# Optimization experiments

Hardware: AMD Instinct MI355X
Metric: run time of the kernel (lower is better)

Reference implementation:

```python
import jax, jax.numpy as jnp
import numpy as np

N, E, Q = 50000, 800000, 2000000   # nodes, edges, quadruplets
F_IN, H, OUT, G = 128, 128, 1, 64  # in_channels, hidden, out_channels, graphs
NRBF = NCBF = NSBF = 6
L = 3  # num_layers


def _mlp2(h, Wa, ba, Wb, bb):
    # Linear -> ReLU -> Linear
    return jax.nn.relu(h @ Wa + ba) @ Wb + bb


def setup_inputs() -> dict:
    key = jax.random.key(0)
    ks = jax.random.split(key, 24)
    s = 0.05
    inp = {
        "x": jax.random.normal(ks[0], (N, F_IN), jnp.float32),
        "rbf": jax.random.normal(ks[1], (E, NRBF), jnp.float32),
        "cbf": jax.random.normal(ks[2], (Q, NCBF), jnp.float32),
        "sbf": jax.random.normal(ks[3], (Q, NSBF), jnp.float32),
        "edge_index": jax.random.randint(ks[4], (2, E), 0, N),
        "l_idx": jax.random.randint(ks[5], (Q,), 0, N),
        "k_idx": jax.random.randint(ks[6], (Q,), 0, E),
        "batch": jnp.sort(jax.random.randint(ks[7], (N,), 0, G)),
        # per-layer params (all layers share shapes since F_IN == H)
        "W_e1a": s * jax.random.normal(ks[8], (L, F_IN + NRBF + NCBF + NSBF, H)),
        "b_e1a": jnp.zeros((L, H)),
        "W_e1b": s * jax.random.normal(ks[9], (L, H, H)),
        "b_e1b": jnp.zeros((L, H)),
        "W_e2a": s * jax.random.normal(ks[10], (L, 2 * H, H)),
        "b_e2a": jnp.zeros((L, H)),
        "W_e2b": s * jax.random.normal(ks[11], (L, H, H)),
        "b_e2b": jnp.zeros((L, H)),
        "W_na": s * jax.random.normal(ks[12], (L, F_IN + H, H)),
        "b_na": jnp.zeros((L, H)),
        "W_nb": s * jax.random.normal(ks[13], (L, H, H)),
        "b_nb": jnp.zeros((L, H)),
        "W_oa": s * jax.random.normal(ks[14], (H, H)),
        "b_oa": jnp.zeros((H,)),
        "W_ob": s * jax.random.normal(ks[15], (H, OUT)),
        "b_ob": jnp.zeros((OUT,)),
    }
    return inp


def reference(x, rbf, cbf, sbf,
              W_e1a, b_e1a, W_e1b, b_e1b,
              W_e2a, b_e2a, W_e2b, b_e2b,
              W_na, b_na, W_nb, b_nb,
              W_oa, b_oa, W_ob, b_ob,
              edge_index, l_idx, k_idx, batch):
    src, dst = edge_index[0], edge_index[1]  # x_j = x[src], index = dst
    h = x
    for p in range(L):
        # quadruplet message: gather-concat-MLP  [Q, F+18] -> [Q, H]
        m_in = jnp.concatenate([h[l_idx], rbf[k_idx], cbf, sbf], axis=-1)
        em = _mlp2(m_in, W_e1a[p], b_e1a[p], W_e1b[p], b_e1b[p])
        # scatter-add quadruplet messages onto edges by k_idx -> [E, H]
        agg_e = jax.ops.segment_sum(em, k_idx, num_segments=E)
        # second stage: per-edge concat (note: aggregated indexed by dst, as in source)
        fin = jnp.concatenate([h[src], agg_e[dst]], axis=-1)
        msg = _mlp2(fin, W_e2a[p], b_e2a[p], W_e2b[p], b_e2b[p])
        # aggregate edge messages to target nodes -> [N, H]
        aggr = jax.ops.segment_sum(msg, dst, num_segments=N)
        h = _mlp2(jnp.concatenate([h, aggr], axis=-1), W_na[p], b_na[p], W_nb[p], b_nb[p])
    # global mean pool over graphs
    counts = jax.ops.segment_sum(jnp.ones((N, 1), h.dtype), batch, num_segments=G)
    pooled = jax.ops.segment_sum(h, batch, num_segments=G) / jnp.maximum(counts, 1.0)
    pooled = jax.nn.relu(pooled)
    return _mlp2(pooled, W_oa, b_oa, W_ob, b_ob)
```

## Files before the change

kernel.cpp:

```cpp
#include <hip/hip_runtime.h>

constexpr int Nn = 50000;
constexpr int Ee = 800000;
constexpr int Qq = 2000000;
constexpr int Gg = 64;
constexpr int Hh = 128;
constexpr int NB64 = (Nn + 63) / 64;
constexpr int NSCB = (Nn + 1023) / 1024;

typedef short bf16x8 __attribute__((ext_vector_type(8)));
typedef float f32x4  __attribute__((ext_vector_type(4)));

__device__ __forceinline__ unsigned short f2bf(float f) {
    unsigned u = __builtin_bit_cast(unsigned, f);
    u += 0x7FFFu + ((u >> 16) & 1u);
    return (unsigned short)(u >> 16);
}
__device__ __forceinline__ float bf2f(unsigned short s) {
    unsigned u = ((unsigned)s) << 16;
    return __builtin_bit_cast(float, u);
}

__global__ void k_hist(const int* __restrict__ idx, int n, int limit,
                       int* __restrict__ hist) {
    int i = blockIdx.x * blockDim.x + threadIdx.x;
    if (i < n) { int v = idx[i]; if (v < limit) atomicAdd(&hist[v], 1); }
}

__global__ __launch_bounds__(1024) void k_scanA(const int* __restrict__ hist,
                                                int* __restrict__ cursor,
                                                int* __restrict__ bsum) {
    __shared__ int s[1024];
    const int tid = threadIdx.x;
    int i = blockIdx.x * 1024 + tid;
    int v = (i < Nn) ? hist[i] : 0;
    s[tid] = v;
    __syncthreads();
    for (int off = 1; off < 1024; off <<= 1) {
        int t = (tid >= off) ? s[tid - off] : 0;
        __syncthreads();
        s[tid] += t;
        __syncthreads();
    }
    if (i < Nn) cursor[i] = s[tid] - v;
    if (tid == 1023) bsum[blockIdx.x] = s[1023];
}
__global__ void k_scanB(int* __restrict__ bsum) {
    __shared__ int s[64];
    const int tid = threadIdx.x;
    int v = (tid < NSCB) ? bsum[tid] : 0;
    s[tid] = v;
    __syncthreads();
    for (int off = 1; off < 64; off <<= 1) {
        int t = (tid >= off) ? s[tid - off] : 0;
        __syncthreads();
        s[tid] += t;
        __syncthreads();
    }
    if (tid < NSCB) bsum[tid] = s[tid] - v;
}
__global__ __launch_bounds__(1024) void k_scanC(int* __restrict__ cursor,
                                                const int* __restrict__ bsum) {
    int i = blockIdx.x * 1024 + threadIdx.x;
    if (i < Nn) cursor[i] += bsum[blockIdx.x];
}

__global__ void k_scatter_e(const int* __restrict__ dst, const int* __restrict__ src,
                            int* __restrict__ cursor, int* __restrict__ srcs) {
    int i = blockIdx.x * blockDim.x + threadIdx.x;
    if (i < Ee) {
        int v = dst[i];
        int p = atomicAdd(&cursor[v], 1);
        srcs[p] = src[i];
    }
}

__global__ void k_scatter_q(const int* __restrict__ k_idx, const int* __restrict__ l_idx,
                            const float* __restrict__ cbf, const float* __restrict__ sbf,
                            int* __restrict__ cursor,
                            int* __restrict__ lq, unsigned short* __restrict__ qfeat) {
    int i = blockIdx.x * blockDim.x + threadIdx.x;
    if (i >= Qq) return;
    int v = k_idx[i];
    if (v >= Nn) return;
    int p = atomicAdd(&cursor[v], 1);
    lq[p] = l_idx[i];
    unsigned short f[12];
#pragma unroll
    for (int k = 0; k < 6; ++k) f[k] = f2bf(cbf[(size_t)i * 6 + k]);
#pragma unroll
    for (int k = 0; k < 6; ++k) f[6 + k] = f2bf(sbf[(size_t)i * 6 + k]);
    *(uint2*)&qfeat[(size_t)p * 12]     = *(uint2*)&f[0];
    *(uint2*)&qfeat[(size_t)p * 12 + 4] = *(uint2*)&f[4];
    *(uint2*)&qfeat[(size_t)p * 12 + 8] = *(uint2*)&f[8];
}

__global__ void k_wtall(const float* __restrict__ We1a0, const float* __restrict__ We1b0,
                        const float* __restrict__ We2a0, const float* __restrict__ We2b0,
                        const float* __restrict__ Wna0,  const float* __restrict__ Wnb0,
                        unsigned short* __restrict__ wbuf) {
    int idx = blockIdx.x * blockDim.x + threadIdx.x;
    if (idx >= 135168) return;
    const int p = blockIdx.y;
    const float* We1a = We1a0 + (size_t)p * 146 * 128;
    const float* We1b = We1b0 + (size_t)p * 128 * 128;
    const float* We2a = We2a0 + (size_t)p * 256 * 128;
    const float* We2b = We2b0 + (size_t)p * 128 * 128;
    const float* Wna  = Wna0  + (size_t)p * 256 * 128;
    const float* Wnb  = Wnb0  + (size_t)p * 128 * 128;
    unsigned short* base = wbuf + (size_t)p * 135168;
    const float* src; int K, Kp, loc;
    if (idx < 16384)       { src = We1a;             K = 128; Kp = 128; loc = idx; }
    else if (idx < 20480)  { src = We1a + 128 * 128; K = 6;   Kp = 32;  loc = idx - 16384; }
    else if (idx < 36864)  { src = We1b;             K = 128; Kp = 128; loc = idx - 20480; }
    else if (idx < 69632)  { src = We2a;             K = 256; Kp = 256; loc = idx - 36864; }
    else if (idx < 86016)  { src = We2b;             K = 128; Kp = 128; loc = idx - 69632; }
    else if (idx < 118784) { src = Wna;              K = 256; Kp = 256; loc = idx - 86016; }
    else                   { src = Wnb;              K = 128; Kp = 128; loc = idx - 118784; }
    int n = loc / Kp, k = loc - n * Kp;
    base[idx] = (k < K) ? f2bf(src[(size_t)k * 128 + n]) : (unsigned short)0;
}

__global__ void k_h0(const float* __restrict__ x, unsigned short* __restrict__ hb) {
    int idx = blockIdx.x * blockDim.x + threadIdx.x;
    if (idx < Nn * Hh) hb[idx] = f2bf(x[idx]);
}

__device__ __forceinline__ void zacc(f32x4 acc[4][2]) {
#pragma unroll
    for (int rt = 0; rt < 4; ++rt)
#pragma unroll
        for (int ct = 0; ct < 2; ++ct)
            acc[rt][ct] = (f32x4){0.f, 0.f, 0.f, 0.f};
}

template<int KK, int SA, int KP>
__device__ __forceinline__ void gemm64(const unsigned short* A,
                                       const unsigned short* __restrict__ Wt,
                                       int k_off, f32x4 acc[4][2]) {
    const int tid = threadIdx.x;
    const int lane = tid & 63;
    const int nb = (tid >> 6) * 32;
    const int rA = lane & 15;
    const int kg = lane >> 4;
#pragma unroll
    for (int ks = 0; ks < KK / 32; ++ks) {
        const int ka = ks * 32 + kg * 8;
        const int kb = k_off + ka;
        bf16x8 b0 = *(const bf16x8*)&Wt[(size_t)(nb + rA) * KP + kb];
        bf16x8 b1 = *(const bf16x8*)&Wt[(size_t)(nb + 16 + rA) * KP + kb];
#pragma unroll
        for (int rt = 0; rt < 4; ++rt) {
            bf16x8 a = *(const bf16x8*)&A[(rt * 16 + rA) * SA + ka];
            acc[rt][0] = __builtin_amdgcn_mfma_f32_16x16x32_bf16(a, b0, acc[rt][0], 0, 0, 0);
            acc[rt][1] = __builtin_amdgcn_mfma_f32_16x16x32_bf16(a, b1, acc[rt][1], 0, 0, 0);
        }
    }
}

__device__ __forceinline__ void store_acc(const f32x4 acc[4][2], unsigned short* out,
                                          int n0, int nmax) {
    const int tid = threadIdx.x;
    const int lane = tid & 63;
    const int nb = (tid >> 6) * 32;
    const int rA = lane & 15, kg = lane >> 4;
#pragma unroll
    for (int rt = 0; rt < 4; ++rt)
#pragma unroll
        for (int ct = 0; ct < 2; ++ct) {
            int col = nb + ct * 16 + rA;
#pragma unroll
            for (int i = 0; i < 4; ++i) {
                int n = n0 + rt * 16 + kg * 4 + i;
                if (n < nmax) out[(size_t)n * 128 + col] = f2bf(acc[rt][ct][i]);
            }
        }
}

__global__ __launch_bounds__(256) void k_pre(
    const unsigned short* __restrict__ hb, const float* __restrict__ rbf,
    const unsigned short* __restrict__ wb,
    unsigned short* __restrict__ P1, unsigned short* __restrict__ Z1,
    unsigned short* __restrict__ P2)
{
    __shared__ unsigned short L[64 * 136];
    const int m0 = blockIdx.x * 64;
    const int tid = threadIdx.x;
    const unsigned short* Wq1t = wb;
    const unsigned short* Wp2t = wb + 16384;
    const unsigned short* We2at = wb + 36864;
    for (int i = tid; i < 64 * 16; i += 256) {
        int row = i >> 4, ch = i & 15;
        int n = min(m0 + row, Nn - 1);
        *(uint4*)&L[row * 136 + ch * 8] = *(const uint4*)&hb[(size_t)n * 128 + ch * 8];
    }
    __syncthreads();
    f32x4 acc[4][2];
    zacc(acc);
    gemm64<128, 136, 128>(L, Wq1t, 0, acc);
    store_acc(acc, P1, m0, Nn);
    zacc(acc);
    gemm64<128, 136, 256>(L, We2at, 0, acc);
    store_acc(acc, Z1, m0, Nn);
    __syncthreads();
    for (int i = tid; i < 64 * 32; i += 256) {
        int row = i >> 5, c = i & 31;
        int n = min(m0 + row, Nn - 1);
        float v = (c < 6) ? rbf[(size_t)n * 6 + c] : 0.f;
        L[row * 136 + c] = f2bf(v);
    }
    __syncthreads();
    zacc(acc);
    gemm64<32, 136, 32>(L, Wp2t, 0, acc);
    store_acc(acc, P2, m0, Nn);
}

__global__ __launch_bounds__(256) void k_quadagg(
    const unsigned short* __restrict__ P1, const unsigned short* __restrict__ P2,
    const unsigned short* __restrict__ qfeat, const int* __restrict__ lq,
    const int* __restrict__ rowend, const int* __restrict__ rowcnt,
    const float* __restrict__ We1a_raw, const float* __restrict__ b_e1a,
    unsigned short* __restrict__ Rb)
{
    __shared__ float W34[12 * 128];
    __shared__ float bia[128];
    const int tid = threadIdx.x;
    for (int i = tid; i < 12 * 128; i += 256) W34[i] = We1a_raw[134 * 128 + i];
    if (tid < 128) bia[tid] = b_e1a[tid];
    __syncthreads();
    const int nd = tid >> 4;
    const int c0 = (tid & 15) * 8;
    const int n = blockIdx.x * 16 + nd;
    const int end = rowend[n];
    const int beg = end - rowcnt[n];
    float base[8];
    {
        uint4 p2v = *(const uint4*)&P2[(size_t)n * 128 + c0];
        const unsigned short* pp = (const unsigned short*)&p2v;
#pragma unroll
        for (int k = 0; k < 8; ++k) base[k] = bia[c0 + k] + bf2f(pp[k]);
    }
    float acc[8];
#pragma unroll
    for (int k = 0; k < 8; ++k) acc[k] = 0.f;
    for (int e = beg; e < end; ++e) {
        int l = lq[e];
        uint4 a = *(const uint4*)&P1[(size_t)l * 128 + c0];
        uint2 f0 = *(const uint2*)&qfeat[(size_t)e * 12];
        uint2 f1 = *(const uint2*)&qfeat[(size_t)e * 12 + 4];
        uint2 f2 = *(const uint2*)&qfeat[(size_t)e * 12 + 8];
        const unsigned short* q0 = (const unsigned short*)&f0;
        const unsigned short* q1 = (const unsigned short*)&f1;
        const unsigned short* q2 = (const unsigned short*)&f2;
        float qv[12] = {bf2f(q0[0]), bf2f(q0[1]), bf2f(q0[2]), bf2f(q0[3]),
                        bf2f(q1[0]), bf2f(q1[1]), bf2f(q1[2]), bf2f(q1[3]),
                        bf2f(q2[0]), bf2f(q2[1]), bf2f(q2[2]), bf2f(q2[3])};
        const unsigned short* ap = (const unsigned short*)&a;
        float t[8];
#pragma unroll
        for (int k = 0; k < 8; ++k) t[k] = base[k] + bf2f(ap[k]);
#pragma unroll
        for (int kk = 0; kk < 12; ++kk) {
            float q_ = qv[kk];
#pragma unroll
            for (int k = 0; k < 8; ++k)
                t[k] = fmaf(q_, W34[kk * 128 + c0 + k], t[k]);
        }
#pragma unroll
        for (int k = 0; k < 8; ++k) acc[k] += fmaxf(t[k], 0.f);
    }
    unsigned short ov[8];
#pragma unroll
    for (int k = 0; k < 8; ++k) ov[k] = f2bf(acc[k]);
    *(uint4*)&Rb[(size_t)n * 128 + c0] = *(uint4*)ov;
}

__global__ __launch_bounds__(256) void k_edgeagg(
    const unsigned short* __restrict__ Z1, const unsigned short* __restrict__ Z2,
    const int* __restrict__ srcs,
    const int* __restrict__ rowend, const int* __restrict__ rowcnt,
    const float* __restrict__ b_e2a,
    unsigned short* __restrict__ Rb)
{
    const int tid = threadIdx.x;
    const int nd = tid >> 4;
    const int c0 = (tid & 15) * 8;
    const int n = blockIdx.x * 16 + nd;
    const int end = rowend[n];
    const int beg = end - rowcnt[n];
    float z2b[8];
    {
        uint4 zv = *(const uint4*)&Z2[(size_t)n * 128 + c0];
        const unsigned short* zp = (const unsigned short*)&zv;
        float4 b0 = *(const float4*)&b_e2a[c0];
        float4 b1 = *(const float4*)&b_e2a[c0 + 4];
        z2b[0] = b0.x + bf2f(zp[0]); z2b[1] = b0.y + bf2f(zp[1]);
        z2b[2] = b0.z + bf2f(zp[2]); z2b[3] = b0.w + bf2f(zp[3]);
        z2b[4] = b1.x + bf2f(zp[4]); z2b[5] = b1.y + bf2f(zp[5]);
        z2b[6] = b1.z + bf2f(zp[6]); z2b[7] = b1.w + bf2f(zp[7]);
    }
    float acc[8];
#pragma unroll
    for (int k = 0; k < 8; ++k) acc[k] = 0.f;
    int e = beg;
    for (; e + 2 <= end; e += 2) {
        int s0 = srcs[e], s1 = srcs[e + 1];
        uint4 a0 = *(const uint4*)&Z1[(size_t)s0 * 128 + c0];
        uint4 a1 = *(const uint4*)&Z1[(size_t)s1 * 128 + c0];
        const unsigned short* p0 = (const unsigned short*)&a0;
        const unsigned short* p1 = (const unsigned short*)&a1;
#pragma unroll
        for (int k = 0; k < 8; ++k) acc[k] += fmaxf(z2b[k] + bf2f(p0[k]), 0.f);
#pragma unroll
        for (int k = 0; k < 8; ++k) acc[k] += fmaxf(z2b[k] + bf2f(p1[k]), 0.f);
    }
    if (e < end) {
        int s0 = srcs[e];
        uint4 a0 = *(const uint4*)&Z1[(size_t)s0 * 128 + c0];
        const unsigned short* p0 = (const unsigned short*)&a0;
#pragma unroll
        for (int k = 0; k < 8; ++k) acc[k] += fmaxf(z2b[k] + bf2f(p0[k]), 0.f);
    }
    unsigned short ov[8];
#pragma unroll
    for (int k = 0; k < 8; ++k) ov[k] = f2bf(acc[k]);
    *(uint4*)&Rb[(size_t)n * 128 + c0] = *(uint4*)ov;
}

__global__ __launch_bounds__(256) void k_agg2z(
    const unsigned short* __restrict__ Rb, const int* __restrict__ cntq,
    const unsigned short* __restrict__ wb, const float* __restrict__ b_e1b,
    unsigned short* __restrict__ Z2)
{
    __shared__ unsigned short L[64 * 136];
    __shared__ int rc[64];
    const int m0 = blockIdx.x * 64;
    const int tid = threadIdx.x;
    const unsigned short* We1bt = wb + 20480;
    const unsigned short* We2at = wb + 36864;
    if (tid < 64) rc[tid] = (m0 + tid < Nn) ? cntq[m0 + tid] : 0;
    for (int i = tid; i < 64 * 16; i += 256) {
        int row = i >> 4, ch = i & 15;
        int n = min(m0 + row, Nn - 1);
        *(uint4*)&L[row * 136 + ch * 8] = *(const uint4*)&Rb[(size_t)n * 128 + ch * 8];
    }
    __syncthreads();
    f32x4 acc[4][2];
    zacc(acc);
    gemm64<128, 136, 128>(L, We1bt, 0, acc);
    __syncthreads();
    {
        const int lane = tid & 63;
        const int nb = (tid >> 6) * 32;
        const int rA = lane & 15, kg = lane >> 4;
#pragma unroll
        for (int rt = 0; rt < 4; ++rt)
#pragma unroll
            for (int ct = 0; ct < 2; ++ct) {
                int col = nb + ct * 16 + rA;
                float bias = b_e1b[col];
#pragma unroll
                for (int i = 0; i < 4; ++i) {
                    int row = rt * 16 + kg * 4 + i;
                    L[row * 136 + col] = f2bf(acc[rt][ct][i] + (float)rc[row] * bias);
                }
            }
    }
    __syncthreads();
    zacc(acc);
    gemm64<128, 136, 256>(L, We2at, 128, acc);
    store_acc(acc, Z2, m0, Nn);
}

__global__ __launch_bounds__(256) void k_nodeNew(
    const unsigned short* __restrict__ Rb, const int* __restrict__ deg,
    const unsigned short* __restrict__ wb,
    const float* __restrict__ b_e2b, const float* __restrict__ b_na,
    const float* __restrict__ b_nb,
    unsigned short* __restrict__ hb)
{
    __shared__ unsigned short L[64 * 136];
    __shared__ int rc[64];
    const int m0 = blockIdx.x * 64;
    const int tid = threadIdx.x;
    const unsigned short* We2bt = wb + 69632;
    const unsigned short* Wnat  = wb + 86016;
    const unsigned short* Wnbt  = wb + 118784;
    const int lane = tid & 63;
    const int nb = (tid >> 6) * 32;
    const int rA = lane & 15, kg = lane >> 4;
    if (tid < 64) rc[tid] = (m0 + tid < Nn) ? deg[m0 + tid] : 0;
    for (int i = tid; i < 64 * 16; i += 256) {
        int row = i >> 4, ch = i & 15;
        int n = min(m0 + row, Nn - 1);
        *(uint4*)&L[row * 136 + ch * 8] = *(const uint4*)&Rb[(size_t)n * 128 + ch * 8];
    }
    __syncthreads();
    f32x4 acc[4][2];
    zacc(acc);
    gemm64<128, 136, 128>(L, We2bt, 0, acc);
    __syncthreads();
#pragma unroll
    for (int rt = 0; rt < 4; ++rt)
#pragma unroll
        for (int ct = 0; ct < 2; ++ct) {
            int col = nb + ct * 16 + rA;
            float bias = b_e2b[col];
#pragma unroll
            for (int i = 0; i < 4; ++i) {
                int row = rt * 16 + kg * 4 + i;
                L[row * 136 + col] = f2bf(acc[rt][ct][i] + (float)rc[row] * bias);
            }
        }
    __syncthreads();
    f32x4 acc2[4][2];
    zacc(acc2);
    gemm64<128, 136, 256>(L, Wnat, 128, acc2);
    __syncthreads();
    for (int i = tid; i < 64 * 16; i += 256) {
        int row = i >> 4, ch = i & 15;
        int n = min(m0 + row, Nn - 1);
        *(uint4*)&L[row * 136 + ch * 8] = *(const uint4*)&hb[(size_t)n * 128 + ch * 8];
    }
    __syncthreads();
    gemm64<128, 136, 256>(L, Wnat, 0, acc2);
    __syncthreads();
#pragma unroll
    for (int rt = 0; rt < 4; ++rt)
#pragma unroll
        for (int ct = 0; ct < 2; ++ct) {
            int col = nb + ct * 16 + rA;
            float bias = b_na[col];
#pragma unroll
            for (int i = 0; i < 4; ++i) {
                int row = rt * 16 + kg * 4 + i;
                L[row * 136 + col] = f2bf(fmaxf(acc2[rt][ct][i] + bias, 0.f));
            }
        }
    __syncthreads();
    zacc(acc);
    gemm64<128, 136, 128>(L, Wnbt, 0, acc);
#pragma unroll
    for (int rt = 0; rt < 4; ++rt)
#pragma unroll
        for (int ct = 0; ct < 2; ++ct) {
            int col = nb + ct * 16 + rA;
            float bias = b_nb[col];
#pragma unroll
            for (int i = 0; i < 4; ++i) {
                int n = m0 + rt * 16 + kg * 4 + i;
                if (n < Nn)
                    hb[(size_t)n * 128 + col] = f2bf(acc[rt][ct][i] + bias);
            }
        }
}

__global__ __launch_bounds__(256) void k_pool(const unsigned short* __restrict__ hb,
                                              const int* __restrict__ batch,
                                              float* __restrict__ pooled,
                                              float* __restrict__ cntg) {
    __shared__ int bseg[200];
    constexpr int CH = 196;
    const int start = blockIdx.x * CH;
    const int end = min(start + CH, Nn);
    if (start >= end) return;
    const int tid = threadIdx.x;
    for (int i = tid; i < end - start; i += 256) bseg[i] = batch[start + i];
    __syncthreads();
    const int j = tid & 127;
    const int rh = tid >> 7;
    float acc = 0.f, cacc = 0.f;
    int cur = -1;
    for (int n = start + rh; n < end; n += 2) {
        int g = bseg[n - start];
        if (g != cur) {
            if (cur >= 0) {
                atomicAdd(&pooled[cur * Hh + j], acc);
                if (j == 0) atomicAdd(&cntg[cur], cacc);
            }
            cur = g; acc = 0.f; cacc = 0.f;
        }
        acc += bf2f(hb[(size_t)n * Hh + j]);
        cacc += 1.f;
    }
    if (cur >= 0) {
        atomicAdd(&pooled[cur * Hh + j], acc);
        if (j == 0) atomicAdd(&cntg[cur], cacc);
    }
}

__global__ __launch_bounds__(128) void k_final(
    const float* __restrict__ pooled, const float* __restrict__ cntg,
    const float* __restrict__ Woa, const float* __restrict__ boa,
    const float* __restrict__ Wob, const float* __restrict__ bob,
    float* __restrict__ out)
{
    __shared__ float p[128];
    __shared__ float t[128];
    __shared__ float red[128];
    const int g = blockIdx.x;
    const int j = threadIdx.x;
    float c = fmaxf(cntg[g], 1.f);
    p[j] = fmaxf(pooled[g * Hh + j] / c, 0.f);
    __syncthreads();
    float acc = boa[j];
    for (int d = 0; d < Hh; ++d) acc = fmaf(p[d], Woa[d * Hh + j], acc);
    t[j] = fmaxf(acc, 0.f);
    __syncthreads();
    red[j] = t[j] * Wob[j];
    __syncthreads();
    for (int s = 64; s > 0; s >>= 1) {
        if (j < s) red[j] += red[j + s];
        __syncthreads();
    }
    if (j == 0) out[g] = red[0] + bob[0];
}

extern "C" void kernel_launch(void* const* d_in, const int* in_sizes, int n_in,
                              void* d_out, int out_size, void* d_ws, size_t ws_size,
                              hipStream_t stream) {
    const float* x     = (const float*)d_in[0];
    const float* rbf   = (const float*)d_in[1];
    const float* cbf   = (const float*)d_in[2];
    const float* sbf   = (const float*)d_in[3];
    const int*   eidx  = (const int*)d_in[4];
    const int*   l_idx = (const int*)d_in[5];
    const int*   k_idx = (const int*)d_in[6];
    const int*   batch = (const int*)d_in[7];
    const float* W_e1a = (const float*)d_in[8];
    const float* b_e1a = (const float*)d_in[9];
    const float* W_e1b = (const float*)d_in[10];
    const float* b_e1b = (const float*)d_in[11];
    const float* W_e2a = (const float*)d_in[12];
    const float* b_e2a = (const float*)d_in[13];
    const float* W_e2b = (const float*)d_in[14];
    const float* b_e2b = (const float*)d_in[15];
    const float* W_na  = (const float*)d_in[16];
    const float* b_na  = (const float*)d_in[17];
    const float* W_nb  = (const float*)d_in[18];
    const float* b_nb  = (const float*)d_in[19];
    const float* W_oa  = (const float*)d_in[20];
    const float* b_oa  = (const float*)d_in[21];
    const float* W_ob  = (const float*)d_in[22];
    const float* b_ob  = (const float*)d_in[23];

    const int* src = eidx;
    const int* dst = eidx + Ee;

    const size_t NHb = (size_t)Nn * Hh * sizeof(unsigned short);
    char* w = (char*)d_ws;
    unsigned short* hb  = (unsigned short*)w; w += NHb;
    unsigned short* P1  = (unsigned short*)w; w += NHb;
    unsigned short* P2  = (unsigned short*)w; w += NHb;
    unsigned short* Z1  = (unsigned short*)w; w += NHb;
    unsigned short* Z2  = (unsigned short*)w; w += NHb;
    unsigned short* Rb  = (unsigned short*)w; w += NHb;
    float* pooled = (float*)w; w += (size_t)Gg * Hh * sizeof(float);
    float* cntg   = (float*)w; w += (size_t)Gg * sizeof(float);
    int*   lq     = (int*)w;   w += (size_t)Qq * sizeof(int);
    unsigned short* qfeat = (unsigned short*)w; w += (size_t)Qq * 12 * sizeof(unsigned short);
    int*   srcs_e = (int*)w;   w += (size_t)Ee * sizeof(int);
    int*   hist_e = (int*)w;   w += (size_t)Nn * sizeof(int);
    int*   hist_q = (int*)w;   w += (size_t)Nn * sizeof(int);
    int*   cur_e  = (int*)w;   w += (size_t)Nn * sizeof(int);
    int*   cur_q  = (int*)w;   w += (size_t)Nn * sizeof(int);
    int*   bsum_e = (int*)w;   w += 64 * sizeof(int);
    int*   bsum_q = (int*)w;   w += 64 * sizeof(int);
    unsigned short* wbuf = (unsigned short*)w;

    const size_t LSTRIDE = 135168;

    hipMemsetAsync(hist_e, 0, Nn * sizeof(int), stream);
    k_hist<<<(Ee + 255) / 256, 256, 0, stream>>>(dst, Ee, Nn, hist_e);
    k_scanA<<<NSCB, 1024, 0, stream>>>(hist_e, cur_e, bsum_e);
    k_scanB<<<1, 64, 0, stream>>>(bsum_e);
    k_scanC<<<NSCB, 1024, 0, stream>>>(cur_e, bsum_e);
    k_scatter_e<<<(Ee + 255) / 256, 256, 0, stream>>>(dst, src, cur_e, srcs_e);
    hipMemsetAsync(hist_q, 0, Nn * sizeof(int), stream);
    k_hist<<<(Qq + 255) / 256, 256, 0, stream>>>(k_idx, Qq, Nn, hist_q);
    k_scanA<<<NSCB, 1024, 0, stream>>>(hist_q, cur_q, bsum_q);
    k_scanB<<<1, 64, 0, stream>>>(bsum_q);
    k_scanC<<<NSCB, 1024, 0, stream>>>(cur_q, bsum_q);
    k_scatter_q<<<(Qq + 255) / 256, 256, 0, stream>>>(k_idx, l_idx, cbf, sbf,
        cur_q, lq, qfeat);

    k_h0<<<(Nn * Hh + 255) / 256, 256, 0, stream>>>(x, hb);

    {
        dim3 g((135168 + 255) / 256, 3);
        k_wtall<<<g, 256, 0, stream>>>(W_e1a, W_e1b, W_e2a, W_e2b, W_na, W_nb, wbuf);
    }

    for (int p = 0; p < 3; ++p) {
        const unsigned short* wb = wbuf + p * LSTRIDE;
        k_pre<<<NB64, 256, 0, stream>>>(hb, rbf, wb, P1, Z1, P2);
        k_quadagg<<<Nn / 16, 256, 0, stream>>>(P1, P2, qfeat, lq,
            cur_q, hist_q, W_e1a + (size_t)p * 146 * 128, b_e1a + (size_t)p * 128, Rb);
        k_agg2z<<<NB64, 256, 0, stream>>>(Rb, hist_q, wb, b_e1b + (size_t)p * 128, Z2);
        k_edgeagg<<<Nn / 16, 256, 0, stream>>>(Z1, Z2, srcs_e, cur_e, hist_e,
            b_e2a + (size_t)p * 128, Rb);
        k_nodeNew<<<NB64, 256, 0, stream>>>(Rb, hist_e, wb,
            b_e2b + (size_t)p * 128, b_na + (size_t)p * 128, b_nb + (size_t)p * 128,
            hb);
    }
    hipMemsetAsync(pooled, 0, (size_t)Gg * Hh * sizeof(float), stream);
    hipMemsetAsync(cntg, 0, (size_t)Gg * sizeof(float), stream);
    k_pool<<<(Nn + 195) / 196, 256, 0, stream>>>(hb, batch, pooled, cntg);
    k_final<<<Gg, 128, 0, stream>>>(pooled, cntg, W_oa, b_oa, W_ob, b_ob, (float*)d_out);
}
```

Baseline: 572.2 us.

## Fuse preprocessing launches and fold next-layer projections into node update kernel

```diff
diff --git a/kernel.cpp b/kernel.cpp
--- a/kernel.cpp
+++ b/kernel.cpp
@@ -21,19 +21,24 @@
     return __builtin_bit_cast(float, u);
 }
 
-__global__ void k_hist(const int* __restrict__ idx, int n, int limit,
-                       int* __restrict__ hist) {
+__global__ void k_hist2(const int* __restrict__ dst, const int* __restrict__ kidx,
+                        int* __restrict__ hist_e, int* __restrict__ hist_q) {
     int i = blockIdx.x * blockDim.x + threadIdx.x;
-    if (i < n) { int v = idx[i]; if (v < limit) atomicAdd(&hist[v], 1); }
-}
-
-__global__ __launch_bounds__(1024) void k_scanA(const int* __restrict__ hist,
-                                                int* __restrict__ cursor,
-                                                int* __restrict__ bsum) {
+    if (i < Ee) atomicAdd(&hist_e[dst[i]], 1);
+    if (i < Qq) { int v = kidx[i]; if (v < Nn) atomicAdd(&hist_q[v], 1); }
+}
+
+__global__ __launch_bounds__(1024) void k_scanA2(const int* __restrict__ he,
+                                                 const int* __restrict__ hq,
+                                                 int* __restrict__ ce, int* __restrict__ cq,
+                                                 int* __restrict__ bs) {
     __shared__ int s[1024];
+    const int* h = blockIdx.y ? hq : he;
+    int* c = blockIdx.y ? cq : ce;
+    int* b = bs + blockIdx.y * 64;
     const int tid = threadIdx.x;
     int i = blockIdx.x * 1024 + tid;
-    int v = (i < Nn) ? hist[i] : 0;
+    int v = (i < Nn) ? h[i] : 0;
     s[tid] = v;
     __syncthreads();
     for (int off = 1; off < 1024; off <<= 1) {
@@ -42,13 +47,14 @@
         s[tid] += t;
         __syncthreads();
     }
-    if (i < Nn) cursor[i] = s[tid] - v;
-    if (tid == 1023) bsum[blockIdx.x] = s[1023];
-}
-__global__ void k_scanB(int* __restrict__ bsum) {
+    if (i < Nn) c[i] = s[tid] - v;
+    if (tid == 1023) b[blockIdx.x] = s[1023];
+}
+__global__ void k_scanB2(int* __restrict__ bs) {
     __shared__ int s[64];
-    const int tid = threadIdx.x;
-    int v = (tid < NSCB) ? bsum[tid] : 0;
+    int* b = bs + blockIdx.x * 64;
+    const int tid = threadIdx.x;
+    int v = (tid < NSCB) ? b[tid] : 0;
     s[tid] = v;
     __syncthreads();
     for (int off = 1; off < 64; off <<= 1) {
@@ -57,42 +63,42 @@
         s[tid] += t;
         __syncthreads();
     }
-    if (tid < NSCB) bsum[tid] = s[tid] - v;
-}
-__global__ __launch_bounds__(1024) void k_scanC(int* __restrict__ cursor,
-                                                const int* __restrict__ bsum) {
+    if (tid < NSCB) b[tid] = s[tid] - v;
+}
+__global__ __launch_bounds__(1024) void k_scanC2(int* __restrict__ ce, int* __restrict__ cq,
+                                                 const int* __restrict__ bs) {
+    int* c = blockIdx.y ? cq : ce;
+    const int* b = bs + blockIdx.y * 64;
     int i = blockIdx.x * 1024 + threadIdx.x;
-    if (i < Nn) cursor[i] += bsum[blockIdx.x];
-}
-
-__global__ void k_scatter_e(const int* __restrict__ dst, const int* __restrict__ src,
-                            int* __restrict__ cursor, int* __restrict__ srcs) {
+    if (i < Nn) c[i] += b[blockIdx.x];
+}
+
+__global__ void k_scatter_both(const int* __restrict__ dst, const int* __restrict__ src,
+                               const int* __restrict__ kidx, const int* __restrict__ lidx,
+                               const float* __restrict__ cbf, const float* __restrict__ sbf,
+                               int* __restrict__ cur_e, int* __restrict__ cur_q,
+                               int* __restrict__ srcs, int* __restrict__ lq,
+                               unsigned short* __restrict__ qfeat) {
     int i = blockIdx.x * blockDim.x + threadIdx.x;
     if (i < Ee) {
-        int v = dst[i];
-        int p = atomicAdd(&cursor[v], 1);
+        int p = atomicAdd(&cur_e[dst[i]], 1);
         srcs[p] = src[i];
     }
-}
-
-__global__ void k_scatter_q(const int* __restrict__ k_idx, const int* __restrict__ l_idx,
-                            const float* __restrict__ cbf, const float* __restrict__ sbf,
-                            int* __restrict__ cursor,
-                            int* __restrict__ lq, unsigned short* __restrict__ qfeat) {
-    int i = blockIdx.x * blockDim.x + threadIdx.x;
-    if (i >= Qq) return;
-    int v = k_idx[i];
-    if (v >= Nn) return;
-    int p = atomicAdd(&cursor[v], 1);
-    lq[p] = l_idx[i];
-    unsigned short f[12];
-#pragma unroll
-    for (int k = 0; k < 6; ++k) f[k] = f2bf(cbf[(size_t)i * 6 + k]);
-#pragma unroll
-    for (int k = 0; k < 6; ++k) f[6 + k] = f2bf(sbf[(size_t)i * 6 + k]);
-    *(uint2*)&qfeat[(size_t)p * 12]     = *(uint2*)&f[0];
-    *(uint2*)&qfeat[(size_t)p * 12 + 4] = *(uint2*)&f[4];
-    *(uint2*)&qfeat[(size_t)p * 12 + 8] = *(uint2*)&f[8];
+    if (i < Qq) {
+        int v = kidx[i];
+        if (v < Nn) {
+            int p = atomicAdd(&cur_q[v], 1);
+            lq[p] = lidx[i];
+            unsigned short f[12];
+#pragma unroll
+            for (int k = 0; k < 6; ++k) f[k] = f2bf(cbf[(size_t)i * 6 + k]);
+#pragma unroll
+            for (int k = 0; k < 6; ++k) f[6 + k] = f2bf(sbf[(size_t)i * 6 + k]);
+            *(uint2*)&qfeat[(size_t)p * 12]     = *(uint2*)&f[0];
+            *(uint2*)&qfeat[(size_t)p * 12 + 4] = *(uint2*)&f[4];
+            *(uint2*)&qfeat[(size_t)p * 12 + 8] = *(uint2*)&f[8];
+        }
+    }
 }
 
 __global__ void k_wtall(const float* __restrict__ We1a0, const float* __restrict__ We1b0,
@@ -121,11 +127,6 @@
     base[idx] = (k < K) ? f2bf(src[(size_t)k * 128 + n]) : (unsigned short)0;
 }
 
-__global__ void k_h0(const float* __restrict__ x, unsigned short* __restrict__ hb) {
-    int idx = blockIdx.x * blockDim.x + threadIdx.x;
-    if (idx < Nn * Hh) hb[idx] = f2bf(x[idx]);
-}
-
 __device__ __forceinline__ void zacc(f32x4 acc[4][2]) {
 #pragma unroll
     for (int rt = 0; rt < 4; ++rt)
@@ -177,42 +178,47 @@
         }
 }
 
-__global__ __launch_bounds__(256) void k_pre(
-    const unsigned short* __restrict__ hb, const float* __restrict__ rbf,
-    const unsigned short* __restrict__ wb,
+__global__ __launch_bounds__(256) void k_pre0(
+    const float* __restrict__ x, const float* __restrict__ rbf,
+    const unsigned short* __restrict__ wbuf,
+    unsigned short* __restrict__ hb,
     unsigned short* __restrict__ P1, unsigned short* __restrict__ Z1,
-    unsigned short* __restrict__ P2)
+    unsigned short* __restrict__ P2all)
 {
-    __shared__ unsigned short L[64 * 136];
+    __shared__ unsigned short TA[64 * 136];
     const int m0 = blockIdx.x * 64;
     const int tid = threadIdx.x;
-    const unsigned short* Wq1t = wb;
-    const unsigned short* Wp2t = wb + 16384;
-    const unsigned short* We2at = wb + 36864;
-    for (int i = tid; i < 64 * 16; i += 256) {
-        int row = i >> 4, ch = i & 15;
-        int n = min(m0 + row, Nn - 1);
-        *(uint4*)&L[row * 136 + ch * 8] = *(const uint4*)&hb[(size_t)n * 128 + ch * 8];
+    for (int i = tid; i < 64 * 32; i += 256) {
+        int row = i >> 5, c = i & 31;
+        int n = m0 + row;
+        int nc = min(n, Nn - 1);
+        float4 v = *(const float4*)&x[(size_t)nc * 128 + c * 4];
+        ushort4 o;
+        o.x = f2bf(v.x); o.y = f2bf(v.y); o.z = f2bf(v.z); o.w = f2bf(v.w);
+        *(ushort4*)&TA[row * 136 + c * 4] = o;
+        if (n < Nn) *(ushort4*)&hb[(size_t)n * 128 + c * 4] = o;
     }
     __syncthreads();
     f32x4 acc[4][2];
     zacc(acc);
-    gemm64<128, 136, 128>(L, Wq1t, 0, acc);
+    gemm64<128, 136, 128>(TA, wbuf, 0, acc);
     store_acc(acc, P1, m0, Nn);
     zacc(acc);
-    gemm64<128, 136, 256>(L, We2at, 0, acc);
+    gemm64<128, 136, 256>(TA, wbuf + 36864, 0, acc);
     store_acc(acc, Z1, m0, Nn);
     __syncthreads();
     for (int i = tid; i < 64 * 32; i += 256) {
         int row = i >> 5, c = i & 31;
-        int n = min(m0 + row, Nn - 1);
-        float v = (c < 6) ? rbf[(size_t)n * 6 + c] : 0.f;
-        L[row * 136 + c] = f2bf(v);
-    }
-    __syncthreads();
-    zacc(acc);
-    gemm64<32, 136, 32>(L, Wp2t, 0, acc);
-    store_acc(acc, P2, m0, Nn);
+        int nc = min(m0 + row, Nn - 1);
+        float v = (c < 6) ? rbf[(size_t)nc * 6 + c] : 0.f;
+        TA[row * 136 + c] = f2bf(v);
+    }
+    __syncthreads();
+    for (int p = 0; p < 3; ++p) {
+        zacc(acc);
+        gemm64<32, 136, 32>(TA, wbuf + (size_t)p * 135168 + 16384, 0, acc);
+        store_acc(acc, P2all + (size_t)p * Nn * 128, m0, Nn);
+    }
 }
 
 __global__ __launch_bounds__(256) void k_quadagg(
@@ -372,12 +378,15 @@
     store_acc(acc, Z2, m0, Nn);
 }
 
+template<int LAST>
 __global__ __launch_bounds__(256) void k_nodeNew(
     const unsigned short* __restrict__ Rb, const int* __restrict__ deg,
     const unsigned short* __restrict__ wb,
     const float* __restrict__ b_e2b, const float* __restrict__ b_na,
     const float* __restrict__ b_nb,
-    unsigned short* __restrict__ hb)
+    unsigned short* __restrict__ hb,
+    const unsigned short* __restrict__ wbn,
+    unsigned short* __restrict__ P1n, unsigned short* __restrict__ Z1n)
 {
     __shared__ unsigned short L[64 * 136];
     __shared__ int rc[64];
@@ -440,6 +449,7 @@
     __syncthreads();
     zacc(acc);
     gemm64<128, 136, 128>(L, Wnbt, 0, acc);
+    __syncthreads();
 #pragma unroll
     for (int rt = 0; rt < 4; ++rt)
 #pragma unroll
@@ -448,11 +458,22 @@
             float bias = b_nb[col];
 #pragma unroll
             for (int i = 0; i < 4; ++i) {
-                int n = m0 + rt * 16 + kg * 4 + i;
-                if (n < Nn)
-                    hb[(size_t)n * 128 + col] = f2bf(acc[rt][ct][i] + bias);
+                int row = rt * 16 + kg * 4 + i;
+                int n = m0 + row;
+                unsigned short hv = f2bf(acc[rt][ct][i] + bias);
+                if (n < Nn) hb[(size_t)n * 128 + col] = hv;
+                if (!LAST) L[row * 136 + col] = hv;
             }
         }
+    if (!LAST) {
+        __syncthreads();
+        zacc(acc);
+        gemm64<128, 136, 128>(L, wbn, 0, acc);
+        store_acc(acc, P1n, m0, Nn);
+        zacc(acc);
+        gemm64<128, 136, 256>(L, wbn + 36864, 0, acc);
+        store_acc(acc, Z1n, m0, Nn);
+    }
 }
 
 __global__ __launch_bounds__(256) void k_pool(const unsigned short* __restrict__ hb,
@@ -549,12 +570,14 @@
 
     const size_t NHb = (size_t)Nn * Hh * sizeof(unsigned short);
     char* w = (char*)d_ws;
-    unsigned short* hb  = (unsigned short*)w; w += NHb;
-    unsigned short* P1  = (unsigned short*)w; w += NHb;
-    unsigned short* P2  = (unsigned short*)w; w += NHb;
-    unsigned short* Z1  = (unsigned short*)w; w += NHb;
-    unsigned short* Z2  = (unsigned short*)w; w += NHb;
-    unsigned short* Rb  = (unsigned short*)w; w += NHb;
+    unsigned short* hb   = (unsigned short*)w; w += NHb;
+    unsigned short* P1a  = (unsigned short*)w; w += NHb;
+    unsigned short* P1b  = (unsigned short*)w; w += NHb;
+    unsigned short* Z1a  = (unsigned short*)w; w += NHb;
+    unsigned short* Z1b  = (unsigned short*)w; w += NHb;
+    unsigned short* Z2   = (unsigned short*)w; w += NHb;
+    unsigned short* Rb   = (unsigned short*)w; w += NHb;
+    unsigned short* P2all = (unsigned short*)w; w += 3 * NHb;
     float* pooled = (float*)w; w += (size_t)Gg * Hh * sizeof(float);
     float* cntg   = (float*)w; w += (size_t)Gg * sizeof(float);
     int*   lq     = (int*)w;   w += (size_t)Qq * sizeof(int);
@@ -564,47 +587,50 @@
     int*   hist_q = (int*)w;   w += (size_t)Nn * sizeof(int);
     int*   cur_e  = (int*)w;   w += (size_t)Nn * sizeof(int);
     int*   cur_q  = (int*)w;   w += (size_t)Nn * sizeof(int);
-    int*   bsum_e = (int*)w;   w += 64 * sizeof(int);
-    int*   bsum_q = (int*)w;   w += 64 * sizeof(int);
+    int*   bsum   = (int*)w;   w += 128 * sizeof(int);
     unsigned short* wbuf = (unsigned short*)w;
 
     const size_t LSTRIDE = 135168;
 
-    hipMemsetAsync(hist_e, 0, Nn * sizeof(int), stream);
-    k_hist<<<(Ee + 255) / 256, 256, 0, stream>>>(dst, Ee, Nn, hist_e);
-    k_scanA<<<NSCB, 1024, 0, stream>>>(hist_e, cur_e, bsum_e);
-    k_scanB<<<1, 64, 0, stream>>>(bsum_e);
-    k_scanC<<<NSCB, 1024, 0, stream>>>(cur_e, bsum_e);
-    k_scatter_e<<<(Ee + 255) / 256, 256, 0, stream>>>(dst, src, cur_e, srcs_e);
-    hipMemsetAsync(hist_q, 0, Nn * sizeof(int), stream);
-    k_hist<<<(Qq + 255) / 256, 256, 0, stream>>>(k_idx, Qq, Nn, hist_q);
-    k_scanA<<<NSCB, 1024, 0, stream>>>(hist_q, cur_q, bsum_q);
-    k_scanB<<<1, 64, 0, stream>>>(bsum_q);
-    k_scanC<<<NSCB, 1024, 0, stream>>>(cur_q, bsum_q);
-    k_scatter_q<<<(Qq + 255) / 256, 256, 0, stream>>>(k_idx, l_idx, cbf, sbf,
-        cur_q, lq, qfeat);
-
-    k_h0<<<(Nn * Hh + 255) / 256, 256, 0, stream>>>(x, hb);
+    hipMemsetAsync(hist_e, 0, 2 * Nn * sizeof(int), stream);
+    k_hist2<<<(Qq + 255) / 256, 256, 0, stream>>>(dst, k_idx, hist_e, hist_q);
+    {
+        dim3 g(NSCB, 2);
+        k_scanA2<<<g, 1024, 0, stream>>>(hist_e, hist_q, cur_e, cur_q, bsum);
+        k_scanB2<<<2, 64, 0, stream>>>(bsum);
+        k_scanC2<<<g, 1024, 0, stream>>>(cur_e, cur_q, bsum);
+    }
+    k_scatter_both<<<(Qq + 255) / 256, 256, 0, stream>>>(dst, src, k_idx, l_idx,
+        cbf, sbf, cur_e, cur_q, srcs_e, lq, qfeat);
 
     {
         dim3 g((135168 + 255) / 256, 3);
         k_wtall<<<g, 256, 0, stream>>>(W_e1a, W_e1b, W_e2a, W_e2b, W_na, W_nb, wbuf);
     }
-
+    k_pre0<<<NB64, 256, 0, stream>>>(x, rbf, wbuf, hb, P1a, Z1a, P2all);
+
+    unsigned short* P1s[2] = { P1a, P1b };
+    unsigned short* Z1s[2] = { Z1a, Z1b };
     for (int p = 0; p < 3; ++p) {
         const unsigned short* wb = wbuf + p * LSTRIDE;
-        k_pre<<<NB64, 256, 0, stream>>>(hb, rbf, wb, P1, Z1, P2);
-        k_quadagg<<<Nn / 16, 256, 0, stream>>>(P1, P2, qfeat, lq,
-            cur_q, hist_q, W_e1a + (size_t)p * 146 * 128, b_e1a + (size_t)p * 128, Rb);
+        const unsigned short* wbn = wbuf + ((p + 1) % 3) * LSTRIDE;
+        int c = p & 1;
+        k_quadagg<<<Nn / 16, 256, 0, stream>>>(P1s[c],
+            P2all + (size_t)p * Nn * 128, qfeat, lq, cur_q, hist_q,
+            W_e1a + (size_t)p * 146 * 128, b_e1a + (size_t)p * 128, Rb);
         k_agg2z<<<NB64, 256, 0, stream>>>(Rb, hist_q, wb, b_e1b + (size_t)p * 128, Z2);
-        k_edgeagg<<<Nn / 16, 256, 0, stream>>>(Z1, Z2, srcs_e, cur_e, hist_e,
+        k_edgeagg<<<Nn / 16, 256, 0, stream>>>(Z1s[c], Z2, srcs_e, cur_e, hist_e,
             b_e2a + (size_t)p * 128, Rb);
-        k_nodeNew<<<NB64, 256, 0, stream>>>(Rb, hist_e, wb,
-            b_e2b + (size_t)p * 128, b_na + (size_t)p * 128, b_nb + (size_t)p * 128,
-            hb);
-    }
-    hipMemsetAsync(pooled, 0, (size_t)Gg * Hh * sizeof(float), stream);
-    hipMemsetAsync(cntg, 0, (size_t)Gg * sizeof(float), stream);
+        if (p < 2)
+            k_nodeNew<0><<<NB64, 256, 0, stream>>>(Rb, hist_e, wb,
+                b_e2b + (size_t)p * 128, b_na + (size_t)p * 128, b_nb + (size_t)p * 128,
+                hb, wbn, P1s[c ^ 1], Z1s[c ^ 1]);
+        else
+            k_nodeNew<1><<<NB64, 256, 0, stream>>>(Rb, hist_e, wb,
+                b_e2b + (size_t)p * 128, b_na + (size_t)p * 128, b_nb + (size_t)p * 128,
+                hb, wbn, P1s[c ^ 1], Z1s[c ^ 1]);
+    }
+    hipMemsetAsync(pooled, 0, (size_t)(Gg * Hh + Gg) * sizeof(float), stream);
     k_pool<<<(Nn + 195) / 196, 256, 0, stream>>>(hb, batch, pooled, cntg);
     k_final<<<Gg, 128, 0, stream>>>(pooled, cntg, W_oa, b_oa, W_ob, b_ob, (float*)d_out);
 }
```

Result: faster. 533.6 us (-6.7%).
